# Kernel optimization log

Hardware: AMD Instinct MI355X
Metric: run time of the kernel (lower is better)

The kernel has to match this reference:

```python
import jax, jax.numpy as jnp
import numpy as np

BIG_NUMBER = 1000000.0
B, N, F, D = 8, 256, 128, 128  # batch, nodes, feat dim, mid/out size


def setup_inputs() -> dict:
    key = jax.random.key(0)
    ks = jax.random.split(key, 16)
    node_fts = jax.random.normal(ks[0], (B, N, F), jnp.float32)
    hidden = jax.random.normal(ks[1], (B, N, F), jnp.float32)
    edge_fts = jax.random.normal(ks[2], (B, N, N, F), jnp.float32)
    e_hidden = jax.random.normal(ks[3], (B, N, N, F), jnp.float32)
    graph_fts = jax.random.normal(ks[4], (B, F), jnp.float32)
    adj_mat = jax.random.randint(ks[5], (B, N, N), 0, 2, jnp.int32)
    s = 0.05
    We = jax.random.normal(ks[6], (2 * F, D), jnp.float32) * s
    be = jnp.zeros((D,), jnp.float32)
    W_m1 = jax.random.normal(ks[7], (2 * F, D), jnp.float32) * s
    b_m1 = jnp.zeros((D,), jnp.float32)
    W_m2 = jax.random.normal(ks[8], (2 * F, D), jnp.float32) * s
    b_m2 = jnp.zeros((D,), jnp.float32)
    W_o1 = jax.random.normal(ks[9], (2 * F, D), jnp.float32) * s
    b_o1 = jnp.zeros((D,), jnp.float32)
    W_o2 = jax.random.normal(ks[10], (D, D), jnp.float32) * s
    b_o2 = jnp.zeros((D,), jnp.float32)
    return dict(node_fts=node_fts, edge_fts=edge_fts, graph_fts=graph_fts,
                adj_mat=adj_mat, hidden=hidden, e_hidden=e_hidden,
                We=We, be=be, W_m1=W_m1, b_m1=b_m1, W_m2=W_m2, b_m2=b_m2,
                W_o1=W_o1, b_o1=b_o1, W_o2=W_o2, b_o2=b_o2)


def reference(node_fts, edge_fts, graph_fts, adj_mat, hidden, e_hidden,
              We, be, W_m1, b_m1, W_m2, b_m2, W_o1, b_o1, W_o2, b_o2):
    # concat node/edge feats with hiddens
    nt = jnp.concatenate([node_fts, hidden], axis=-1)            # [B,N,2F]
    et = jnp.concatenate([edge_fts, e_hidden], axis=-1) @ We + be  # [B,N,N,D]
    # append virtual node (zeros features, fully connected)
    nt = jnp.concatenate([nt, jnp.zeros((B, 1, 2 * F), nt.dtype)], axis=1)  # [B,N+1,2F]
    adj = adj_mat.astype(nt.dtype)
    adj = jnp.concatenate([adj, jnp.ones((B, 1, N), nt.dtype)], axis=1)
    adj = jnp.concatenate([adj, jnp.ones((B, N + 1, 1), nt.dtype)], axis=2)  # [B,N+1,N+1]
    # MPNN layer (reduction = max)
    msg_1 = nt @ W_m1 + b_m1  # [B,N+1,D]
    msg_2 = nt @ W_m2 + b_m2  # [B,N+1,D]
    msgs = msg_1[:, None, :, :] + msg_2[:, :, None, :]  # [B,N+1,N+1,D]
    msgs = jnp.where(adj[..., None] > 0, msgs, -BIG_NUMBER)
    msgs = jnp.max(msgs, axis=1)  # [B,N+1,D]
    ret = (nt @ W_o1 + b_o1) + (msgs @ W_o2 + b_o2)  # [B,N+1,D]
    # strip virtual node; padded edge tensor sliced back equals et
    return ret[:, :N, :], et
```

## Files before the change

### kernel.cpp

```cpp
#include <hip/hip_runtime.h>
#include <hip/hip_bf16.h>

#define Bn 8
#define Nn 256
#define Fn 128
#define Dn 128

typedef __bf16 bf16_t;
typedef bf16_t bf16x8 __attribute__((ext_vector_type(8)));
typedef float f32x4 __attribute__((ext_vector_type(4)));

__global__ __launch_bounds__(512, 4) void mfma_gemm_kernel(
    const float* __restrict__ edge, const float* __restrict__ ehid,
    const float* __restrict__ We,   const float* __restrict__ be,
    const float* __restrict__ node, const float* __restrict__ hidden,
    const float* __restrict__ W_m1, const float* __restrict__ b_m1,
    const float* __restrict__ W_m2, const float* __restrict__ b_m2,
    const float* __restrict__ W_o1, const float* __restrict__ b_o1,
    float* __restrict__ out_et,
    float* __restrict__ ws_m1, float* __restrict__ ws_m2, float* __restrict__ ws_h1)
{
    __shared__ __align__(16) bf16_t lds[128 * 256];

    const int t = threadIdx.x;

    const float *X1, *X2, *W, *bias;
    float* out;
    long rowbase;
    bool streaming;
    if (blockIdx.x < 2048) {
        X1 = edge; X2 = ehid; W = We; bias = be; out = out_et;
        rowbase = (long)blockIdx.x * 256;
        streaming = true;
    } else {
        const int e = blockIdx.x - 2048;
        const int w = e >> 3;
        rowbase = (long)(e & 7) * 256;
        X1 = node; X2 = hidden;
        streaming = false;
        if (w == 0)      { W = W_m2; bias = b_m2; out = ws_m2; }
        else if (w == 1) { W = W_m1; bias = b_m1; out = ws_m1; }
        else             { W = W_o1; bias = b_o1; out = ws_h1; }
    }

    {
        const int kb = t >> 4;
        const int g  = t & 15;
        const float* wp = W + (kb * 8) * 128 + g * 8;
        float buf[8][8];
        #pragma unroll
        for (int r = 0; r < 8; ++r) {
            f32x4 u0 = *(const f32x4*)(wp + r * 128);
            f32x4 u1 = *(const f32x4*)(wp + r * 128 + 4);
            buf[r][0] = u0[0]; buf[r][1] = u0[1]; buf[r][2] = u0[2]; buf[r][3] = u0[3];
            buf[r][4] = u1[0]; buf[r][5] = u1[1]; buf[r][6] = u1[2]; buf[r][7] = u1[3];
        }
        #pragma unroll
        for (int j = 0; j < 8; ++j) {
            const int n  = g * 8 + j;
            const int cp = kb ^ j ^ (g & 7);
            bf16x8 w8;
            #pragma unroll
            for (int r = 0; r < 8; ++r) w8[r] = (bf16_t)buf[r][j];
            *(bf16x8*)(&lds[n * 256 + cp * 8]) = w8;
        }
    }
    __syncthreads();

    const int wv     = t >> 6;
    const int l      = t & 63;
    const int lane16 = l & 15;
    const int quad   = l >> 4;

    float bev[8];
    #pragma unroll
    for (int nt = 0; nt < 8; ++nt) bev[nt] = bias[nt * 16 + lane16];

    const long wrow = rowbase + wv * 32;

    const float* base1 = X1 + (wrow + lane16) * 128 + quad * 8;
    const float* base2 = X2 + (wrow + lane16) * 128 + quad * 8;

    #define CHUNK_PTR(s, c) (((c) < 4 ? base1 : base2) + (s) * 16 * 128 + ((c) & 3) * 32)

    f32x4 u0[2], u1[2];
    { const float* p = CHUNK_PTR(0, 0); u0[0] = *(const f32x4*)p; u1[0] = *(const f32x4*)(p + 4); }
    { const float* p = CHUNK_PTR(0, 1); u0[1] = *(const f32x4*)p; u1[1] = *(const f32x4*)(p + 4); }

    f32x4 acc[8];
    #pragma unroll
    for (int nt = 0; nt < 8; ++nt) acc[nt] = (f32x4){0.f, 0.f, 0.f, 0.f};

    #pragma unroll
    for (int cc = 0; cc < 16; ++cc) {
        const int s  = cc >> 3;
        const int c  = cc & 7;
        const int pb = cc & 1;

        bf16x8 afrag;
        #pragma unroll
        for (int j = 0; j < 4; ++j) {
            afrag[j]     = (bf16_t)u0[pb][j];
            afrag[j + 4] = (bf16_t)u1[pb][j];
        }

        if (cc + 2 < 16) {
            const int s2 = (cc + 2) >> 3, c2 = (cc + 2) & 7;
            const float* p = CHUNK_PTR(s2, c2);
            u0[pb] = *(const f32x4*)p;
            u1[pb] = *(const f32x4*)(p + 4);
        }

        #pragma unroll
        for (int nt = 0; nt < 8; ++nt) {
            const int n    = nt * 16 + lane16;
            const int cidx = c * 4 + quad;
            const int cp   = cidx ^ (n & 7) ^ ((n >> 3) & 7);
            bf16x8 bfrag = *(const bf16x8*)(&lds[n * 256 + cp * 8]);
            acc[nt] = __builtin_amdgcn_mfma_f32_16x16x32_bf16(afrag, bfrag, acc[nt], 0, 0, 0);
        }

        if (c == 7) {
            const long orow0 = wrow + s * 16 + quad * 4;
            #pragma unroll
            for (int nt = 0; nt < 8; ++nt) {
                #pragma unroll
                for (int r = 0; r < 4; ++r) {
                    const float v = acc[nt][r] + bev[nt];
                    float* p = out + (orow0 + r) * 128 + nt * 16 + lane16;
                    if (streaming) __builtin_nontemporal_store(v, p);
                    else           *p = v;
                }
            }
            #pragma unroll
            for (int nt = 0; nt < 8; ++nt) acc[nt] = (f32x4){0.f, 0.f, 0.f, 0.f};
        }
    }
    #undef CHUNK_PTR
}

__global__ __launch_bounds__(256) void ret_kernel(
    const int* __restrict__ adj,
    const float* __restrict__ m2, const float* __restrict__ m1,
    const float* __restrict__ h1,
    const float* __restrict__ W_o2, const float* __restrict__ b_o2,
    const float* __restrict__ b_m2,
    float* __restrict__ out)
{
    __shared__ int   adjc[256];
    __shared__ float part[8][128];
    __shared__ float sv[128];

    const int bj = blockIdx.x;
    const int b  = bj >> 8;
    const int j  = bj & 255;
    const int t  = threadIdx.x;

    adjc[t] = adj[(b * 256 + t) * 256 + j];
    __syncthreads();

    const int s  = t >> 5;
    const int dg = t & 31;
    f32x4 mx4;
    mx4[0] = mx4[1] = mx4[2] = mx4[3] = -3.0e38f;
    const float* m2p = m2 + ((long)b * 256 + s * 32) * 128 + dg * 4;
    #pragma unroll 8
    for (int i = 0; i < 32; ++i) {
        const f32x4 v = *(const f32x4*)(m2p + i * 128);
        const bool on = (adjc[s * 32 + i] != 0);
        mx4[0] = on ? fmaxf(mx4[0], v[0]) : mx4[0];
        mx4[1] = on ? fmaxf(mx4[1], v[1]) : mx4[1];
        mx4[2] = on ? fmaxf(mx4[2], v[2]) : mx4[2];
        mx4[3] = on ? fmaxf(mx4[3], v[3]) : mx4[3];
    }
    *(f32x4*)&part[s][dg * 4] = mx4;
    __syncthreads();

    if (t < 128) {
        float m = b_m2[t];
        #pragma unroll
        for (int ss = 0; ss < 8; ++ss) m = fmaxf(m, part[ss][t]);
        sv[t] = m1[bj * 128 + t] + m;
    }
    __syncthreads();

    const int d = t & 127;
    const int h = t >> 7;
    float r = 0.f;
    const float* wp = W_o2 + (h * 64) * 128 + d;
    #pragma unroll 8
    for (int k = 0; k < 64; ++k)
        r += sv[h * 64 + k] * wp[k * 128];

    if (h == 1) part[0][d] = r;
    __syncthreads();
    if (h == 0)
        out[bj * 128 + d] = r + part[0][d] + h1[bj * 128 + d] + b_o2[d];
}

extern "C" void kernel_launch(void* const* d_in, const int* in_sizes, int n_in,
                              void* d_out, int out_size, void* d_ws, size_t ws_size,
                              hipStream_t stream)
{
    const float* node   = (const float*)d_in[0];
    const float* edge   = (const float*)d_in[1];
    const int*   adj    = (const int*)d_in[3];
    const float* hidden = (const float*)d_in[4];
    const float* ehid   = (const float*)d_in[5];
    const float* We     = (const float*)d_in[6];
    const float* be     = (const float*)d_in[7];
    const float* W_m1   = (const float*)d_in[8];
    const float* b_m1   = (const float*)d_in[9];
    const float* W_m2   = (const float*)d_in[10];
    const float* b_m2   = (const float*)d_in[11];
    const float* W_o1   = (const float*)d_in[12];
    const float* b_o1   = (const float*)d_in[13];
    const float* W_o2   = (const float*)d_in[14];
    const float* b_o2   = (const float*)d_in[15];

    float* out_ret = (float*)d_out;
    float* out_et  = (float*)d_out + Bn * Nn * Dn;

    float* ws_m2 = (float*)d_ws;
    float* ws_m1 = ws_m2 + 2048 * 128;
    float* ws_h1 = ws_m1 + 2048 * 128;

    hipLaunchKernelGGL(mfma_gemm_kernel, dim3(2048 + 24), dim3(512), 0, stream,
                       edge, ehid, We, be, node, hidden,
                       W_m1, b_m1, W_m2, b_m2, W_o1, b_o1,
                       out_et, ws_m1, ws_m2, ws_h1);
    hipLaunchKernelGGL(ret_kernel, dim3(2048), dim3(256), 0, stream,
                       adj, ws_m2, ws_m1, ws_h1, W_o2, b_o2, b_m2, out_ret);
}
```

Before: 672.3 us.

## Stage A tiles via async global_load_lds with 1024-thread blocks

Activation rows now stream straight from global memory into swizzled LDS buffers through global_load_lds, double-buffered per wave with explicit vmcnt waits, replacing the register prefetch. Blocks grow to 1024 threads with each wave covering 16 rows instead of 32. The small node GEMM blocks are moved to the front of the grid. The weight transpose is split so more threads share it. LDS use doubles to 128KB per block, which limits occupancy to one block per CU. The hand-placed waitcnt and barriers are fragile.

After: 643.4 us. 4.3% less time.

```diff
diff --git a/kernel.cpp b/kernel.cpp
--- a/kernel.cpp
+++ b/kernel.cpp
@@ -8,9 +8,14 @@
 
 typedef __bf16 bf16_t;
 typedef bf16_t bf16x8 __attribute__((ext_vector_type(8)));
+typedef bf16_t bf16x4 __attribute__((ext_vector_type(4)));
 typedef float f32x4 __attribute__((ext_vector_type(4)));
 
-__global__ __launch_bounds__(512, 4) void mfma_gemm_kernel(
+#define GLOAD16(g, l) __builtin_amdgcn_global_load_lds(                        \
+    (const __attribute__((address_space(1))) void*)(g),                        \
+    (__attribute__((address_space(3))) void*)(l), 16, 0, 0)
+
+__global__ __launch_bounds__(1024, 4) void mfma_gemm_kernel(
     const float* __restrict__ edge, const float* __restrict__ ehid,
     const float* __restrict__ We,   const float* __restrict__ be,
     const float* __restrict__ node, const float* __restrict__ hidden,
@@ -20,7 +25,9 @@
     float* __restrict__ out_et,
     float* __restrict__ ws_m1, float* __restrict__ ws_m2, float* __restrict__ ws_h1)
 {
-    __shared__ __align__(16) bf16_t lds[128 * 256];
+    __shared__ __align__(16) char smem[131072];
+    bf16_t* wlds = (bf16_t*)smem;
+    float*  albs = (float*)(smem + 65536);
 
     const int t = threadIdx.x;
 
@@ -28,115 +35,123 @@
     float* out;
     long rowbase;
     bool streaming;
-    if (blockIdx.x < 2048) {
+    if (blockIdx.x >= 24) {
         X1 = edge; X2 = ehid; W = We; bias = be; out = out_et;
-        rowbase = (long)blockIdx.x * 256;
+        rowbase = (long)(blockIdx.x - 24) * 256;
         streaming = true;
     } else {
-        const int e = blockIdx.x - 2048;
+        const int e = blockIdx.x;
         const int w = e >> 3;
         rowbase = (long)(e & 7) * 256;
-        X1 = node; X2 = hidden;
-        streaming = false;
+        X1 = node; X2 = hidden; streaming = false;
         if (w == 0)      { W = W_m2; bias = b_m2; out = ws_m2; }
         else if (w == 1) { W = W_m1; bias = b_m1; out = ws_m1; }
         else             { W = W_o1; bias = b_o1; out = ws_h1; }
     }
-
-    {
-        const int kb = t >> 4;
-        const int g  = t & 15;
-        const float* wp = W + (kb * 8) * 128 + g * 8;
-        float buf[8][8];
-        #pragma unroll
-        for (int r = 0; r < 8; ++r) {
-            f32x4 u0 = *(const f32x4*)(wp + r * 128);
-            f32x4 u1 = *(const f32x4*)(wp + r * 128 + 4);
-            buf[r][0] = u0[0]; buf[r][1] = u0[1]; buf[r][2] = u0[2]; buf[r][3] = u0[3];
-            buf[r][4] = u1[0]; buf[r][5] = u1[1]; buf[r][6] = u1[2]; buf[r][7] = u1[3];
-        }
-        #pragma unroll
-        for (int j = 0; j < 8; ++j) {
-            const int n  = g * 8 + j;
-            const int cp = kb ^ j ^ (g & 7);
-            bf16x8 w8;
-            #pragma unroll
-            for (int r = 0; r < 8; ++r) w8[r] = (bf16_t)buf[r][j];
-            *(bf16x8*)(&lds[n * 256 + cp * 8]) = w8;
-        }
-    }
-    __syncthreads();
 
     const int wv     = t >> 6;
     const int l      = t & 63;
     const int lane16 = l & 15;
     const int quad   = l >> 4;
 
+    const long wrow = rowbase + wv * 16;
+
+    const int arow0 = l >> 3;
+    const int akg   = (l & 7) ^ (arow0 & 7);
+    const float* aX1 = X1 + (wrow + arow0) * 128 + akg * 4;
+    const float* aX2 = X2 + (wrow + arow0) * 128 + akg * 4;
+    float* abw = albs + wv * 1024;
+
+#define ISSUE_CHUNK(c_, b_) do {                                              \
+        const float* s_ = ((c_) < 4) ? (aX1 + (c_) * 32)                      \
+                                     : (aX2 + ((c_) - 4) * 32);               \
+        float* d_ = abw + (b_) * 512;                                         \
+        GLOAD16(s_,        d_);                                               \
+        GLOAD16(s_ + 1024, d_ + 256);             \
+    } while (0)
+
+    ISSUE_CHUNK(0, 0);
+    ISSUE_CHUNK(1, 1);
+
+    {
+        const int kb4 = t >> 4;
+        const int g   = t & 15;
+        const int k0  = kb4 * 4;
+        const float* wp = W + (long)k0 * 128 + g * 8;
+        f32x4 a0[4], a1[4];
+        #pragma unroll
+        for (int r = 0; r < 4; ++r) {
+            a0[r] = *(const f32x4*)(wp + r * 128);
+            a1[r] = *(const f32x4*)(wp + r * 128 + 4);
+        }
+        #pragma unroll
+        for (int j = 0; j < 8; ++j) {
+            const int n  = g * 8 + j;
+            const int cp = (kb4 >> 1) ^ j ^ (g & 7);
+            bf16x4 v;
+            #pragma unroll
+            for (int r = 0; r < 4; ++r)
+                v[r] = (bf16_t)(j < 4 ? a0[r][j] : a1[r][j - 4]);
+            *(bf16x4*)(&wlds[n * 256 + cp * 8 + (k0 & 7)]) = v;
+        }
+    }
+    __syncthreads();
+
     float bev[8];
     #pragma unroll
     for (int nt = 0; nt < 8; ++nt) bev[nt] = bias[nt * 16 + lane16];
 
-    const long wrow = rowbase + wv * 32;
-
-    const float* base1 = X1 + (wrow + lane16) * 128 + quad * 8;
-    const float* base2 = X2 + (wrow + lane16) * 128 + quad * 8;
-
-    #define CHUNK_PTR(s, c) (((c) < 4 ? base1 : base2) + (s) * 16 * 128 + ((c) & 3) * 32)
-
-    f32x4 u0[2], u1[2];
-    { const float* p = CHUNK_PTR(0, 0); u0[0] = *(const f32x4*)p; u1[0] = *(const f32x4*)(p + 4); }
-    { const float* p = CHUNK_PTR(0, 1); u0[1] = *(const f32x4*)p; u1[1] = *(const f32x4*)(p + 4); }
-
     f32x4 acc[8];
     #pragma unroll
     for (int nt = 0; nt < 8; ++nt) acc[nt] = (f32x4){0.f, 0.f, 0.f, 0.f};
 
-    #pragma unroll
-    for (int cc = 0; cc < 16; ++cc) {
-        const int s  = cc >> 3;
-        const int c  = cc & 7;
-        const int pb = cc & 1;
-
+    const int kst0 = (quad * 2)     ^ (lane16 & 7);
+    const int kst1 = (quad * 2 + 1) ^ (lane16 & 7);
+
+    #pragma unroll
+    for (int c = 0; c < 8; ++c) {
+        const int b = c & 1;
+
+        if (c < 7) asm volatile("s_waitcnt vmcnt(2)" ::: "memory");
+        else       asm volatile("s_waitcnt vmcnt(0)" ::: "memory");
+        __builtin_amdgcn_sched_barrier(0);
+
+        const float* bufp = abw + b * 512 + lane16 * 32;
+        f32x4 u0 = *(const f32x4*)(bufp + kst0 * 4);
+        f32x4 u1 = *(const f32x4*)(bufp + kst1 * 4);
         bf16x8 afrag;
         #pragma unroll
         for (int j = 0; j < 4; ++j) {
-            afrag[j]     = (bf16_t)u0[pb][j];
-            afrag[j + 4] = (bf16_t)u1[pb][j];
-        }
-
-        if (cc + 2 < 16) {
-            const int s2 = (cc + 2) >> 3, c2 = (cc + 2) & 7;
-            const float* p = CHUNK_PTR(s2, c2);
-            u0[pb] = *(const f32x4*)p;
-            u1[pb] = *(const f32x4*)(p + 4);
-        }
+            afrag[j]     = (bf16_t)u0[j];
+            afrag[j + 4] = (bf16_t)u1[j];
+        }
+
+        asm volatile("s_waitcnt lgkmcnt(0)" ::: "memory");
+        __builtin_amdgcn_sched_barrier(0);
+        if (c + 2 < 8) ISSUE_CHUNK(c + 2, b);
 
         #pragma unroll
         for (int nt = 0; nt < 8; ++nt) {
             const int n    = nt * 16 + lane16;
             const int cidx = c * 4 + quad;
             const int cp   = cidx ^ (n & 7) ^ ((n >> 3) & 7);
-            bf16x8 bfrag = *(const bf16x8*)(&lds[n * 256 + cp * 8]);
+            bf16x8 bfrag = *(const bf16x8*)(&wlds[n * 256 + cp * 8]);
             acc[nt] = __builtin_amdgcn_mfma_f32_16x16x32_bf16(afrag, bfrag, acc[nt], 0, 0, 0);
         }
-
-        if (c == 7) {
-            const long orow0 = wrow + s * 16 + quad * 4;
-            #pragma unroll
-            for (int nt = 0; nt < 8; ++nt) {
-                #pragma unroll
-                for (int r = 0; r < 4; ++r) {
-                    const float v = acc[nt][r] + bev[nt];
-                    float* p = out + (orow0 + r) * 128 + nt * 16 + lane16;
-                    if (streaming) __builtin_nontemporal_store(v, p);
-                    else           *p = v;
-                }
-            }
-            #pragma unroll
-            for (int nt = 0; nt < 8; ++nt) acc[nt] = (f32x4){0.f, 0.f, 0.f, 0.f};
-        }
-    }
-    #undef CHUNK_PTR
+    }
+#undef ISSUE_CHUNK
+
+    const long orow0 = wrow + quad * 4;
+    #pragma unroll
+    for (int nt = 0; nt < 8; ++nt) {
+        #pragma unroll
+        for (int r = 0; r < 4; ++r) {
+            const float v = acc[nt][r] + bev[nt];
+            float* p = out + (orow0 + r) * 128 + nt * 16 + lane16;
+            if (streaming) __builtin_nontemporal_store(v, p);
+            else           *p = v;
+        }
+    }
 }
 
 __global__ __launch_bounds__(256) void ret_kernel(
@@ -225,7 +240,7 @@
     float* ws_m1 = ws_m2 + 2048 * 128;
     float* ws_h1 = ws_m1 + 2048 * 128;
 
-    hipLaunchKernelGGL(mfma_gemm_kernel, dim3(2048 + 24), dim3(512), 0, stream,
+    hipLaunchKernelGGL(mfma_gemm_kernel, dim3(2048 + 24), dim3(1024), 0, stream,
                        edge, ehid, We, be, node, hidden,
                        W_m1, b_m1, W_m2, b_m2, W_o1, b_o1,
                        out_et, ws_m1, ws_m2, ws_h1);
```
